# Performance work log

Hardware: AMD Instinct MI355X
Metric: run time of the kernel (lower is better)

Reference implementation:

```python
import jax, jax.numpy as jnp
import numpy as np
import math

B, S, E, H = 2, 4096, 1024, 16
W = 256  # one-sided attention window (attention_window // 2)


def setup_inputs() -> dict:
    key = jax.random.key(0)
    ks = jax.random.split(key, 7)
    init = lambda k, shp: jax.random.normal(k, shp, jnp.float32) * 0.02
    return {
        "hidden_states": jax.random.normal(ks[0], (B, S, E), jnp.float32),
        "attention_mask": jnp.zeros((B, S), jnp.int32),  # 0 = local attention
        "q_w": init(ks[1], (E, E)), "q_b": jnp.zeros((E,), jnp.float32),
        "k_w": init(ks[2], (E, E)), "k_b": jnp.zeros((E,), jnp.float32),
        "v_w": init(ks[3], (E, E)), "v_b": jnp.zeros((E,), jnp.float32),
    }


def _banded_attention(hidden_states, attention_mask, q_w, q_b, k_w, k_b, v_w, v_b):
    D = E // H          # head dim
    w = W               # one-sided window
    nc = S // w         # number of query chunks of length w
    # Projections (torch Linear: x @ W.T + b); query pre-scaled by sqrt(head_dim)
    q = (hidden_states @ q_w.T + q_b) / math.sqrt(D)
    k = hidden_states @ k_w.T + k_b
    v = hidden_states @ v_w.T + v_b
    heads = lambda x: x.reshape(B, S, H, D).transpose(0, 2, 1, 3)  # [B,H,S,D]
    q, k, v = heads(q), heads(k), heads(v)

    qc = q.reshape(B, H, nc, w, D)                       # [B,H,nc,w,D]
    pad = lambda x: jnp.pad(x, ((0, 0), (0, 0), (w, w), (0, 0)))
    # chunk c of keys/values covers padded positions [c*w, c*w + 3w)
    idx = (jnp.arange(nc) * w)[:, None] + jnp.arange(3 * w)[None, :]  # [nc,3w]
    kc = pad(k)[:, :, idx]                               # [B,H,nc,3w,D]
    vc = pad(v)[:, :, idx]                               # [B,H,nc,3w,D]

    # banded scores: query x in chunk attends padded key y; rel offset = y-w-x
    scores = jnp.einsum('bhcxd,bhcyd->bhcxy', qc, kc)    # [B,H,nc,w,3w]

    # additive mask from attention_mask (!=0 -> -10000 at that key position)
    fm = jnp.where(attention_mask != 0, -10000.0, 0.0)   # [B,S]
    fmc = jnp.pad(fm, ((0, 0), (w, w)))[:, idx]          # [B,nc,3w]
    scores = scores + fmc[:, None, :, None, :]

    # validity: |rel| <= w (the 2w+1 band) and key index j in [0, S)
    x = jnp.arange(w)[:, None]                           # [w,1]
    y = jnp.arange(3 * w)[None, :]                       # [1,3w]
    rel = y - w - x                                      # [w,3w]
    j = (jnp.arange(nc) * w)[:, None, None] + (y - w)[None]  # [nc,1,3w] key idx
    valid = (jnp.abs(rel) <= w)[None] & (j >= 0) & (j < S)   # [nc,w,3w]
    scores = jnp.where(valid[None, None], scores, -jnp.inf)

    probs = jax.nn.softmax(scores.astype(jnp.float32), axis=-1)
    ctx = jnp.einsum('bhcxy,bhcyd->bhcxd', probs, vc)    # [B,H,nc,w,D]
    return ctx.reshape(B, H, S, D).transpose(0, 2, 1, 3).reshape(B, S, E)


def reference(hidden_states, attention_mask, q_w, q_b, k_w, k_b, v_w, v_b):
    return _banded_attention(hidden_states, attention_mask,
                             q_w, q_b, k_w, k_b, v_w, v_b)
```

## Files before the change

kernel.cpp:

```cpp
#include <hip/hip_runtime.h>
#include <math.h>

constexpr int Bn  = 2;
constexpr int Sn  = 4096;
constexpr int En  = 1024;
constexpr int Hn  = 16;
constexpr int Mtot = Bn * Sn;
constexpr int Kp  = 1024;
constexpr int PAD = 72;

typedef __bf16    bf16x8 __attribute__((ext_vector_type(8)));
typedef __bf16    bf16x4 __attribute__((ext_vector_type(4)));
typedef _Float16  f16x8  __attribute__((ext_vector_type(8)));
typedef _Float16  f16x4  __attribute__((ext_vector_type(4)));
typedef float     f32x4  __attribute__((ext_vector_type(4)));

__global__ void __launch_bounds__(256)
cvt_hs_kernel(const float* __restrict__ hs, _Float16* __restrict__ hs16)
{
    int t = blockIdx.x * 256 + threadIdx.x;
    int m = t >> 8;
    int k = (t & 255) << 2;
    float4 x = *(const float4*)&hs[((size_t)m << 10) + k];
    f16x4 h;
    h[0] = (_Float16)x.x; h[1] = (_Float16)x.y;
    h[2] = (_Float16)x.z; h[3] = (_Float16)x.w;
    *(f16x4*)&hs16[((size_t)m << 10) + k] = h;
}

__global__ void __launch_bounds__(256)
cvt_w_kernel(const float* __restrict__ qw, const float* __restrict__ kw,
             const float* __restrict__ vw, _Float16* __restrict__ w16)
{
    int t = blockIdx.x * 256 + threadIdx.x;
    int gn = t >> 8;
    int k  = (t & 255) << 2;
    int p  = gn >> 10, n = gn & 1023;
    const float* src = (p == 0) ? qw : (p == 1) ? kw : vw;
    float4 x = *(const float4*)&src[((size_t)n << 10) + k];
    f16x4 h;
    h[0] = (_Float16)x.x; h[1] = (_Float16)x.y;
    h[2] = (_Float16)x.z; h[3] = (_Float16)x.w;
    *(f16x4*)&w16[((size_t)gn << 10) + k] = h;
}

__device__ inline void load_lds16(const void* g, void* s) {
    __builtin_amdgcn_global_load_lds((const __attribute__((address_space(1))) void*)g,
                                     (__attribute__((address_space(3))) void*)s,
                                     16, 0, 0);
}

__device__ inline void block_sync() {
    asm volatile("" ::: "memory");
    __builtin_amdgcn_s_barrier();
    asm volatile("" ::: "memory");
}
__device__ inline void vm_wait8() { asm volatile("s_waitcnt vmcnt(8)" ::: "memory"); }
__device__ inline void vm_wait4() { asm volatile("s_waitcnt vmcnt(4)" ::: "memory"); }
__device__ inline void vm_wait0() { asm volatile("s_waitcnt vmcnt(0)" ::: "memory"); }

template<int PM>
__global__ void __launch_bounds__(512, 2)
qkv_mfma_kernel(const _Float16* __restrict__ A2, const _Float16* __restrict__ B2,
                const float* __restrict__ qb, const float* __restrict__ kb,
                const float* __restrict__ vb,
                __bf16* __restrict__ q16, __bf16* __restrict__ k16,
                __bf16* __restrict__ vt16, int n0base)
{
    __shared__ _Float16 As[2][2][256][32];
    __shared__ _Float16 Bs[2][2][256][32];

    const int tid  = threadIdx.x;
    const int w    = tid >> 6;
    const int lane = tid & 63;
    const int wm   = w >> 2, wn = w & 3;
    const int mrow = lane & 15, quad = lane >> 4;
    const int m0   = blockIdx.x * 256;
    const int n0   = n0base + blockIdx.y * 256;

    const int subrow = lane >> 2;
    const int gch    = ((lane & 3) ^ ((lane >> 3) & 3)) * 8;
    const _Float16* Ag = A2 + (size_t)(m0 + w * 32 + subrow) * Kp + gch;
    const _Float16* Bg = B2 + (size_t)(n0 + w * 32 + subrow) * Kp + gch;

    const int sl = (quad ^ ((mrow >> 1) & 3)) * 8;

    f32x4 acc[8][4] = {};

    auto stageA = [&](int kt, int bi, int kc) {
        const size_t goff = (size_t)kt * 64 + kc * 32;
#pragma unroll
        for (int l = 0; l < 2; l++)
            load_lds16(Ag + (size_t)l * 16 * Kp + goff, &As[bi][kc][w * 32 + l * 16][0]);
    };
    auto stageB = [&](int kt, int bi, int kc) {
        const size_t goff = (size_t)kt * 64 + kc * 32;
#pragma unroll
        for (int l = 0; l < 2; l++)
            load_lds16(Bg + (size_t)l * 16 * Kp + goff, &Bs[bi][kc][w * 32 + l * 16][0]);
    };
    auto ladder = [&](const f16x8* AF, const f16x8* BF, int r0) {
        __builtin_amdgcn_s_setprio(1);
#pragma unroll
        for (int ti = 0; ti < 4; ti++)
#pragma unroll
            for (int tj = 0; tj < 4; tj++) {
                if (PM == 0)
                    acc[r0 + ti][tj] = __builtin_amdgcn_mfma_f32_16x16x32_f16(
                        BF[tj], AF[ti], acc[r0 + ti][tj], 0, 0, 0);
                else
                    acc[r0 + ti][tj] = __builtin_amdgcn_mfma_f32_16x16x32_f16(
                        AF[ti], BF[tj], acc[r0 + ti][tj], 0, 0, 0);
            }
        __builtin_amdgcn_s_setprio(0);
    };

    constexpr int NT = Kp / 64;

    float4 bv4[4];
    const int p = n0 >> 10;
    {
        const float* bptr = (p == 0) ? qb : (p == 1) ? kb : vb;
#pragma unroll
        for (int tj = 0; tj < 4; tj++) {
            if (PM == 0) {
                const int fl = (n0 + wn * 64 + tj * 16 + quad * 4) & 1023;
                bv4[tj] = *(const float4*)&bptr[fl];
            } else {
                const int n = (n0 + wn * 64 + tj * 16 + mrow) & 1023;
                bv4[tj].x = bptr[n];
            }
        }
    }

    stageA(0, 0, 0); stageB(0, 0, 0);
    stageA(0, 0, 1); stageB(0, 0, 1);
    vm_wait4();
    block_sync();

    for (int kt = 0; kt < NT; ++kt) {
        const int rb = kt & 1, wb = rb ^ 1;
        const bool pre  = (kt + 1 < NT);
        const bool last = (kt + 1 == NT);
        f16x8 af[4], bf[4];

#pragma unroll
        for (int t = 0; t < 4; t++)
            af[t] = *(const f16x8*)&As[rb][0][wm * 128 + t * 16 + mrow][sl];
#pragma unroll
        for (int t = 0; t < 4; t++)
            bf[t] = *(const f16x8*)&Bs[rb][0][wn * 64 + t * 16 + mrow][sl];
        if (pre) { stageA(kt + 1, wb, 0); stageB(kt + 1, wb, 0); }
        block_sync();
        ladder(af, bf, 0);
        block_sync();

#pragma unroll
        for (int t = 0; t < 4; t++)
            af[t] = *(const f16x8*)&As[rb][0][wm * 128 + 64 + t * 16 + mrow][sl];
        if (pre) { stageA(kt + 1, wb, 1); stageB(kt + 1, wb, 1); }
        block_sync();
        ladder(af, bf, 4);
        if (last) vm_wait0(); else vm_wait8();
        block_sync();

#pragma unroll
        for (int t = 0; t < 4; t++)
            af[t] = *(const f16x8*)&As[rb][1][wm * 128 + t * 16 + mrow][sl];
#pragma unroll
        for (int t = 0; t < 4; t++)
            bf[t] = *(const f16x8*)&Bs[rb][1][wn * 64 + t * 16 + mrow][sl];
        block_sync();
        ladder(af, bf, 0);
        block_sync();

#pragma unroll
        for (int t = 0; t < 4; t++)
            af[t] = *(const f16x8*)&As[rb][1][wm * 128 + 64 + t * 16 + mrow][sl];
        block_sync();
        ladder(af, bf, 4);
        vm_wait4();
        block_sync();
    }

    if (PM == 0) {
        __bf16* dst = (p == 0) ? q16 : k16;
        const float scl = (p == 0) ? 0.125f : 1.0f;
#pragma unroll
        for (int ti = 0; ti < 8; ti++) {
            const int m  = m0 + wm * 128 + ti * 16 + mrow;
            const int bb = m >> 12, ss = m & 4095;
#pragma unroll
            for (int tj = 0; tj < 4; tj++) {
                const int fl = (n0 + wn * 64 + tj * 16 + quad * 4) & 1023;
                const int hh = fl >> 6, dd = fl & 63;
                bf16x4 o;
                o[0] = (__bf16)((acc[ti][tj][0] + bv4[tj].x) * scl);
                o[1] = (__bf16)((acc[ti][tj][1] + bv4[tj].y) * scl);
                o[2] = (__bf16)((acc[ti][tj][2] + bv4[tj].z) * scl);
                o[3] = (__bf16)((acc[ti][tj][3] + bv4[tj].w) * scl);
                *(bf16x4*)&dst[((size_t)(bb * Hn + hh) * Sn + ss) * 64 + dd] = o;
            }
        }
    } else {
#pragma unroll
        for (int tj = 0; tj < 4; tj++) {
            const int n  = n0 + wn * 64 + tj * 16 + mrow;
            const float bv = bv4[tj].x;
            const int hh = (n & 1023) >> 6, dd = n & 63;
#pragma unroll
            for (int ti = 0; ti < 8; ti++) {
                const int m  = m0 + wm * 128 + ti * 16 + quad * 4;
                const int bb = m >> 12, ss = m & 4095;
                bf16x4 pv4;
#pragma unroll
                for (int r = 0; r < 4; r++)
                    pv4[r] = (__bf16)(acc[ti][tj][r] + bv);
                *(bf16x4*)&vt16[((size_t)(bb * Hn + hh) * 64 + dd) * Sn + ss] = pv4;
            }
        }
    }
}

__global__ void __launch_bounds__(256, 2)
banded_attn_kernel(const __bf16* __restrict__ q16, const __bf16* __restrict__ k16,
                   const __bf16* __restrict__ vt16, const int* __restrict__ mask,
                   float* __restrict__ out)
{
    __shared__ __bf16 Kt[2][64 * PAD];
    __shared__ __bf16 Vt[2][64 * PAD];
    __shared__ __bf16 Pt[4][64 * PAD];
    __shared__ float  Msh[768];

    const int c = blockIdx.x, h = blockIdx.y, b = blockIdx.z;
    const int bh = b * Hn + h;
    const int i0 = c * 256;
    const int jwin0 = i0 - 256;
    const int tid  = threadIdx.x;
    const int wv   = tid >> 6;
    const int lane = tid & 63;
    const int quad = lane >> 4, mrow = lane & 15;

#pragma unroll
    for (int rep = 0; rep < 3; rep++) {
        int idx = rep * 256 + tid;
        int jg  = jwin0 + idx;
        float mv = 0.f;
        if (jg >= 0 && jg < Sn && mask[b * Sn + jg] != 0) mv = -10000.f;
        Msh[idx] = mv;
    }

    bf16x8 qf[4][2];
    const __bf16* qbase = q16 + (((size_t)bh * Sn + i0 + wv * 64) << 6);
#pragma unroll
    for (int tjq = 0; tjq < 4; tjq++)
#pragma unroll
        for (int kc = 0; kc < 2; kc++)
            qf[tjq][kc] = *(const bf16x8*)(qbase + (16 * tjq + mrow) * 64 + 32 * kc + 8 * quad);

    const int sr = lane >> 3;
    const int sc = lane & 7;
    bf16x8 kreg0, kreg1, vreg0, vreg1;
    auto gload = [&](int st) {
        const int j0 = jwin0 + st * 64;
        const int r0 = wv * 16 + sr;
        const int r1 = wv * 16 + 8 + sr;
        int jk0 = j0 + r0; jk0 = jk0 < 0 ? 0 : (jk0 > Sn - 1 ? Sn - 1 : jk0);
        int jk1 = j0 + r1; jk1 = jk1 < 0 ? 0 : (jk1 > Sn - 1 ? Sn - 1 : jk1);
        kreg0 = *(const bf16x8*)&k16[(((size_t)bh * Sn + jk0) << 6) + sc * 8];
        kreg1 = *(const bf16x8*)&k16[(((size_t)bh * Sn + jk1) << 6) + sc * 8];
        int jv = j0 + sc * 8; jv = jv < 0 ? 0 : (jv > Sn - 8 ? Sn - 8 : jv);
        vreg0 = *(const bf16x8*)&vt16[((size_t)bh * 64 + r0) * Sn + jv];
        vreg1 = *(const bf16x8*)&vt16[((size_t)bh * 64 + r1) * Sn + jv];
    };
    auto swrite = [&](int buf) {
        *(bf16x8*)&Kt[buf][(wv * 16 + sr) * PAD + sc * 8]     = kreg0;
        *(bf16x8*)&Kt[buf][(wv * 16 + 8 + sr) * PAD + sc * 8] = kreg1;
        *(bf16x8*)&Vt[buf][(wv * 16 + sr) * PAD + sc * 8]     = vreg0;
        *(bf16x8*)&Vt[buf][(wv * 16 + 8 + sr) * PAD + sc * 8] = vreg1;
    };

    f32x4 acc_o[4][4] = {};
    float lrun[4] = {0.f, 0.f, 0.f, 0.f};
    __bf16* Pw = &Pt[wv][0];

    gload(0);
    swrite(0);
    __syncthreads();

    for (int st = 0; st < 12; st++) {
        const int buf = st & 1;
        if (st + 1 < 12) gload(st + 1);

        if (st >= wv && st <= wv + 8) {
            const __bf16* KtB = &Kt[buf][0];
            const __bf16* VtB = &Vt[buf][0];
#pragma unroll
            for (int ti = 0; ti < 4; ti++) {
                bf16x8 ak0 = *(const bf16x8*)&KtB[(16 * ti + mrow) * PAD + quad * 8];
                bf16x8 ak1 = *(const bf16x8*)&KtB[(16 * ti + mrow) * PAD + 32 + quad * 8];
                const int y0 = 64 * st + 16 * ti + 4 * quad;
                f32x4 ms4 = *(const f32x4*)&Msh[y0];
#pragma unroll
                for (int tjq = 0; tjq < 4; tjq++) {
                    f32x4 s = {};
                    s = __builtin_amdgcn_mfma_f32_16x16x32_bf16(ak0, qf[tjq][0], s, 0, 0, 0);
                    s = __builtin_amdgcn_mfma_f32_16x16x32_bf16(ak1, qf[tjq][1], s, 0, 0, 0);
                    const int xq = 64 * wv + 16 * tjq + mrow;
                    bf16x4 pk;
                    float psum = 0.f;
#pragma unroll
                    for (int r = 0; r < 4; r++) {
                        const int y = y0 + r;
                        bool ok = ((unsigned)(y - xq) <= 512u) &
                                  ((unsigned)(jwin0 + y) < 4096u);
                        float pv = ok ? __expf(s[r] + ms4[r]) : 0.f;
                        psum += pv;
                        pk[r] = (__bf16)pv;
                    }
                    lrun[tjq] += psum;
                    *(bf16x4*)&Pw[(16 * tjq + mrow) * PAD + 16 * ti + 4 * quad] = pk;
                }
            }
#pragma unroll
            for (int kc2 = 0; kc2 < 2; kc2++) {
                bf16x8 av[4];
#pragma unroll
                for (int dt = 0; dt < 4; dt++)
                    av[dt] = *(const bf16x8*)&VtB[(16 * dt + mrow) * PAD + kc2 * 32 + quad * 8];
#pragma unroll
                for (int tjq = 0; tjq < 4; tjq++) {
                    bf16x8 pf = *(const bf16x8*)&Pw[(16 * tjq + mrow) * PAD + kc2 * 32 + quad * 8];
#pragma unroll
                    for (int dt = 0; dt < 4; dt++)
                        acc_o[dt][tjq] = __builtin_amdgcn_mfma_f32_16x16x32_bf16(
                            av[dt], pf, acc_o[dt][tjq], 0, 0, 0);
                }
            }
        }

        if (st + 1 < 12) {
            swrite((st + 1) & 1);
            __syncthreads();
        }
    }

    float inv[4];
#pragma unroll
    for (int tjq = 0; tjq < 4; tjq++) {
        float l = lrun[tjq];
        l += __shfl_xor(l, 16);
        l += __shfl_xor(l, 32);
        inv[tjq] = 1.0f / l;
    }
#pragma unroll
    for (int dt = 0; dt < 4; dt++)
#pragma unroll
        for (int tjq = 0; tjq < 4; tjq++) {
            f32x4 o = acc_o[dt][tjq];
            o[0] *= inv[tjq]; o[1] *= inv[tjq]; o[2] *= inv[tjq]; o[3] *= inv[tjq];
            float* dst = out + ((size_t)(b * Sn + i0 + wv * 64 + 16 * tjq + mrow)) * En
                             + h * 64 + 16 * dt + 4 * quad;
            *(f32x4*)dst = o;
        }
}

extern "C" void kernel_launch(void* const* d_in, const int* in_sizes, int n_in,
                              void* d_out, int out_size, void* d_ws, size_t ws_size,
                              hipStream_t stream) {
    const float* hs  = (const float*)d_in[0];
    const int*  mask = (const int*)d_in[1];
    const float* qw  = (const float*)d_in[2];
    const float* qb  = (const float*)d_in[3];
    const float* kw  = (const float*)d_in[4];
    const float* kb  = (const float*)d_in[5];
    const float* vw  = (const float*)d_in[6];
    const float* vb  = (const float*)d_in[7];
    float* out = (float*)d_out;

    _Float16* hs16 = (_Float16*)d_ws;
    _Float16* w16  = (_Float16*)((char*)d_ws + (size_t)16777216);
    __bf16*   q16  = (__bf16*)((char*)d_ws + (size_t)23068672);
    __bf16*   k16  = (__bf16*)((char*)d_ws + (size_t)39845888);
    __bf16*   vt16 = (__bf16*)((char*)d_ws + (size_t)56623104);

    cvt_hs_kernel<<<8192, 256, 0, stream>>>(hs, hs16);
    cvt_w_kernel <<<3072, 256, 0, stream>>>(qw, kw, vw, w16);

    dim3 pgridQK(Mtot / 256, 2048 / 256);
    qkv_mfma_kernel<0><<<pgridQK, 512, 0, stream>>>(hs16, w16, qb, kb, vb,
                                                    q16, k16, vt16, 0);
    dim3 pgridV(Mtot / 256, 1024 / 256);
    qkv_mfma_kernel<1><<<pgridV, 512, 0, stream>>>(hs16, w16, qb, kb, vb,
                                                   q16, k16, vt16, 2048);

    dim3 agrid(Sn / 256, Hn, Bn);
    banded_attn_kernel<<<agrid, 256, 0, stream>>>(q16, k16, vt16, mask, out);
}
```

Baseline: 225.0 us.

## Merge conversion and QKV projection launches, fold mask into MFMA init

Merges the two fp32-to-fp16 conversion kernels into one launch and the separate QK and V projection GEMM launches into one 12-column grid that branches on blockIdx.y. This removes launch overhead and the tail gaps between back-to-back kernels. In the attention kernel, the key-mask bias now seeds the MFMA accumulator, and out-of-range keys get -10000 in shared memory instead of an explicit index check. The band check runs only on the two edge stages, so interior tiles skip per-element comparisons. The trade-off is that out-of-range keys now contribute exp(s-10000), which underflows to zero, rather than being excluded exactly.

```diff
diff --git a/kernel.cpp b/kernel.cpp
--- a/kernel.cpp
+++ b/kernel.cpp
@@ -16,32 +16,33 @@
 typedef float     f32x4  __attribute__((ext_vector_type(4)));
 
 __global__ void __launch_bounds__(256)
-cvt_hs_kernel(const float* __restrict__ hs, _Float16* __restrict__ hs16)
+cvt_all_kernel(const float* __restrict__ hs,
+               const float* __restrict__ qw, const float* __restrict__ kw,
+               const float* __restrict__ vw,
+               _Float16* __restrict__ hs16, _Float16* __restrict__ w16)
 {
-    int t = blockIdx.x * 256 + threadIdx.x;
-    int m = t >> 8;
-    int k = (t & 255) << 2;
-    float4 x = *(const float4*)&hs[((size_t)m << 10) + k];
-    f16x4 h;
-    h[0] = (_Float16)x.x; h[1] = (_Float16)x.y;
-    h[2] = (_Float16)x.z; h[3] = (_Float16)x.w;
-    *(f16x4*)&hs16[((size_t)m << 10) + k] = h;
-}
-
-__global__ void __launch_bounds__(256)
-cvt_w_kernel(const float* __restrict__ qw, const float* __restrict__ kw,
-             const float* __restrict__ vw, _Float16* __restrict__ w16)
-{
-    int t = blockIdx.x * 256 + threadIdx.x;
-    int gn = t >> 8;
-    int k  = (t & 255) << 2;
-    int p  = gn >> 10, n = gn & 1023;
-    const float* src = (p == 0) ? qw : (p == 1) ? kw : vw;
-    float4 x = *(const float4*)&src[((size_t)n << 10) + k];
-    f16x4 h;
-    h[0] = (_Float16)x.x; h[1] = (_Float16)x.y;
-    h[2] = (_Float16)x.z; h[3] = (_Float16)x.w;
-    *(f16x4*)&w16[((size_t)gn << 10) + k] = h;
+    const int bid = blockIdx.x;
+    if (bid < 8192) {
+        int t = bid * 256 + threadIdx.x;
+        int m = t >> 8;
+        int k = (t & 255) << 2;
+        float4 x = *(const float4*)&hs[((size_t)m << 10) + k];
+        f16x4 h;
+        h[0] = (_Float16)x.x; h[1] = (_Float16)x.y;
+        h[2] = (_Float16)x.z; h[3] = (_Float16)x.w;
+        *(f16x4*)&hs16[((size_t)m << 10) + k] = h;
+    } else {
+        int t = (bid - 8192) * 256 + threadIdx.x;
+        int gn = t >> 8;
+        int k  = (t & 255) << 2;
+        int p  = gn >> 10, n = gn & 1023;
+        const float* src = (p == 0) ? qw : (p == 1) ? kw : vw;
+        float4 x = *(const float4*)&src[((size_t)n << 10) + k];
+        f16x4 h;
+        h[0] = (_Float16)x.x; h[1] = (_Float16)x.y;
+        h[2] = (_Float16)x.z; h[3] = (_Float16)x.w;
+        *(f16x4*)&w16[((size_t)gn << 10) + k] = h;
+    }
 }
 
 __device__ inline void load_lds16(const void* g, void* s) {
@@ -59,24 +60,23 @@
 __device__ inline void vm_wait4() { asm volatile("s_waitcnt vmcnt(4)" ::: "memory"); }
 __device__ inline void vm_wait0() { asm volatile("s_waitcnt vmcnt(0)" ::: "memory"); }
 
+typedef _Float16 ldsAB_t[2][2][256][32];
+
 template<int PM>
-__global__ void __launch_bounds__(512, 2)
-qkv_mfma_kernel(const _Float16* __restrict__ A2, const _Float16* __restrict__ B2,
-                const float* __restrict__ qb, const float* __restrict__ kb,
-                const float* __restrict__ vb,
-                __bf16* __restrict__ q16, __bf16* __restrict__ k16,
-                __bf16* __restrict__ vt16, int n0base)
+__device__ __forceinline__ void
+qkv_body(ldsAB_t& As, ldsAB_t& Bs,
+         const _Float16* __restrict__ A2, const _Float16* __restrict__ B2,
+         const float* __restrict__ qb, const float* __restrict__ kb,
+         const float* __restrict__ vb,
+         __bf16* __restrict__ q16, __bf16* __restrict__ k16,
+         __bf16* __restrict__ vt16, int n0)
 {
-    __shared__ _Float16 As[2][2][256][32];
-    __shared__ _Float16 Bs[2][2][256][32];
-
     const int tid  = threadIdx.x;
     const int w    = tid >> 6;
     const int lane = tid & 63;
     const int wm   = w >> 2, wn = w & 3;
     const int mrow = lane & 15, quad = lane >> 4;
     const int m0   = blockIdx.x * 256;
-    const int n0   = n0base + blockIdx.y * 256;
 
     const int subrow = lane >> 2;
     const int gch    = ((lane & 3) ^ ((lane >> 3) & 3)) * 8;
@@ -222,6 +222,22 @@
     }
 }
 
+__global__ void __launch_bounds__(512, 2)
+qkv_fused_kernel(const _Float16* __restrict__ A2, const _Float16* __restrict__ B2,
+                 const float* __restrict__ qb, const float* __restrict__ kb,
+                 const float* __restrict__ vb,
+                 __bf16* __restrict__ q16, __bf16* __restrict__ k16,
+                 __bf16* __restrict__ vt16)
+{
+    __shared__ ldsAB_t As, Bs;
+    const int by = blockIdx.y;
+    if (by < 8)
+        qkv_body<0>(As, Bs, A2, B2, qb, kb, vb, q16, k16, vt16, by * 256);
+    else
+        qkv_body<1>(As, Bs, A2, B2, qb, kb, vb, q16, k16, vt16,
+                    2048 + (by - 8) * 256);
+}
+
 __global__ void __launch_bounds__(256, 2)
 banded_attn_kernel(const __bf16* __restrict__ q16, const __bf16* __restrict__ k16,
                    const __bf16* __restrict__ vt16, const int* __restrict__ mask,
@@ -245,8 +261,9 @@
     for (int rep = 0; rep < 3; rep++) {
         int idx = rep * 256 + tid;
         int jg  = jwin0 + idx;
-        float mv = 0.f;
-        if (jg >= 0 && jg < Sn && mask[b * Sn + jg] != 0) mv = -10000.f;
+        float mv = -10000.f;
+        if (jg >= 0 && jg < Sn)
+            mv = (mask[b * Sn + jg] != 0) ? -10000.f : 0.f;
         Msh[idx] = mv;
     }
 
@@ -295,28 +312,36 @@
         if (st >= wv && st <= wv + 8) {
             const __bf16* KtB = &Kt[buf][0];
             const __bf16* VtB = &Vt[buf][0];
+            const bool edge = (st == wv) || (st == wv + 8);
 #pragma unroll
             for (int ti = 0; ti < 4; ti++) {
                 bf16x8 ak0 = *(const bf16x8*)&KtB[(16 * ti + mrow) * PAD + quad * 8];
                 bf16x8 ak1 = *(const bf16x8*)&KtB[(16 * ti + mrow) * PAD + 32 + quad * 8];
                 const int y0 = 64 * st + 16 * ti + 4 * quad;
-                f32x4 ms4 = *(const f32x4*)&Msh[y0];
+                const f32x4 ms4 = *(const f32x4*)&Msh[y0];
 #pragma unroll
                 for (int tjq = 0; tjq < 4; tjq++) {
-                    f32x4 s = {};
+                    f32x4 s = ms4;
                     s = __builtin_amdgcn_mfma_f32_16x16x32_bf16(ak0, qf[tjq][0], s, 0, 0, 0);
                     s = __builtin_amdgcn_mfma_f32_16x16x32_bf16(ak1, qf[tjq][1], s, 0, 0, 0);
-                    const int xq = 64 * wv + 16 * tjq + mrow;
                     bf16x4 pk;
                     float psum = 0.f;
-#pragma unroll
-                    for (int r = 0; r < 4; r++) {
-                        const int y = y0 + r;
-                        bool ok = ((unsigned)(y - xq) <= 512u) &
-                                  ((unsigned)(jwin0 + y) < 4096u);
-                        float pv = ok ? __expf(s[r] + ms4[r]) : 0.f;
-                        psum += pv;
-                        pk[r] = (__bf16)pv;
+                    if (edge) {
+                        const int xq = 64 * wv + 16 * tjq + mrow;
+#pragma unroll
+                        for (int r = 0; r < 4; r++) {
+                            bool ok = ((unsigned)(y0 + r - xq) <= 512u);
+                            float pv = ok ? __expf(s[r]) : 0.f;
+                            psum += pv;
+                            pk[r] = (__bf16)pv;
+                        }
+                    } else {
+#pragma unroll
+                        for (int r = 0; r < 4; r++) {
+                            float pv = __expf(s[r]);
+                            psum += pv;
+                            pk[r] = (__bf16)pv;
+                        }
                     }
                     lrun[tjq] += psum;
                     *(bf16x4*)&Pw[(16 * tjq + mrow) * PAD + 16 * ti + 4 * quad] = pk;
@@ -384,15 +409,11 @@
     __bf16*   k16  = (__bf16*)((char*)d_ws + (size_t)39845888);
     __bf16*   vt16 = (__bf16*)((char*)d_ws + (size_t)56623104);
 
-    cvt_hs_kernel<<<8192, 256, 0, stream>>>(hs, hs16);
-    cvt_w_kernel <<<3072, 256, 0, stream>>>(qw, kw, vw, w16);
-
-    dim3 pgridQK(Mtot / 256, 2048 / 256);
-    qkv_mfma_kernel<0><<<pgridQK, 512, 0, stream>>>(hs16, w16, qb, kb, vb,
-                                                    q16, k16, vt16, 0);
-    dim3 pgridV(Mtot / 256, 1024 / 256);
-    qkv_mfma_kernel<1><<<pgridV, 512, 0, stream>>>(hs16, w16, qb, kb, vb,
-                                                   q16, k16, vt16, 2048);
+    cvt_all_kernel<<<8192 + 3072, 256, 0, stream>>>(hs, qw, kw, vw, hs16, w16);
+
+    dim3 pgrid(Mtot / 256, 12);
+    qkv_fused_kernel<<<pgrid, 512, 0, stream>>>(hs16, w16, qb, kb, vb,
+                                                q16, k16, vt16);
 
     dim3 agrid(Sn / 256, Hn, Bn);
     banded_attn_kernel<<<agrid, 256, 0, stream>>>(q16, k16, vt16, mask, out);
```

Result: no change. 220.8 us (-1.9%).
